# Kernel optimization log

Hardware: AMD Instinct MI355X
Metric: run time of the kernel (lower is better)

The kernel has to match this reference:

```python
import jax, jax.numpy as jnp
import numpy as np

E = 64      # embedding_dim
H = 64      # h_dim
MLP = 1024  # mlp_dim (attention hidden)
PRE1 = 512  # mlp_pre_pool hidden
BNK = 1024  # bottleneck_dim
S = 256     # num scenes (equal-size groups replacing seq_start_end)
P = 16      # pedestrians per scene
B = S * P   # total batch of pedestrians
T = 8       # obs_len for vx/vy (only last row used)
EPS = 1e-5  # BatchNorm eps


def _bn(x, g, b, m, v):
    # eval-mode BatchNorm1d over the last (feature) axis
    return (x - m) * jax.lax.rsqrt(v + EPS) * g + b


def setup_inputs() -> dict:
    key = jax.random.key(0)
    ks = jax.random.split(key, 24)
    def n(k, shape, s=1.0):
        return jax.random.normal(k, shape, jnp.float32) * s
    return {
        "h_states": n(ks[0], (1, B, H)),
        "end_pos": n(ks[1], (B, 2)),
        "vx": n(ks[2], (T, B)),
        "vy": n(ks[3], (T, B)),
        "W_sp": n(ks[4], (2, E), 0.05), "b_sp": jnp.zeros((E,), jnp.float32),
        "W_vel": n(ks[5], (2, E), 0.05), "b_vel": jnp.zeros((E,), jnp.float32),
        "Wa1": n(ks[6], (2 * E, MLP), 0.05), "ba1": jnp.zeros((MLP,), jnp.float32),
        "ga1": jnp.ones((MLP,), jnp.float32), "bta1": jnp.zeros((MLP,), jnp.float32),
        "ma1": n(ks[7], (MLP,), 0.1), "va1": jax.random.uniform(ks[8], (MLP,), jnp.float32) + 0.5,
        "Wa2": n(ks[9], (MLP, 1), 0.05), "ba2": jnp.zeros((1,), jnp.float32),
        "ga2": jnp.ones((1,), jnp.float32), "bta2": jnp.zeros((1,), jnp.float32),
        "ma2": n(ks[10], (1,), 0.1), "va2": jax.random.uniform(ks[11], (1,), jnp.float32) + 0.5,
        "Wp1": n(ks[12], (E + H, PRE1), 0.05), "bp1": jnp.zeros((PRE1,), jnp.float32),
        "gp1": jnp.ones((PRE1,), jnp.float32), "btp1": jnp.zeros((PRE1,), jnp.float32),
        "mp1": n(ks[13], (PRE1,), 0.1), "vp1": jax.random.uniform(ks[14], (PRE1,), jnp.float32) + 0.5,
        "Wp2": n(ks[15], (PRE1, BNK), 0.05), "bp2": jnp.zeros((BNK,), jnp.float32),
        "gp2": jnp.ones((BNK,), jnp.float32), "btp2": jnp.zeros((BNK,), jnp.float32),
        "mp2": n(ks[16], (BNK,), 0.1), "vp2": jax.random.uniform(ks[17], (BNK,), jnp.float32) + 0.5,
        "num_scenes": S, "num_ped": P,
    }


def _forward(h_states, end_pos, vx, vy, W_sp, b_sp, W_vel, b_vel,
             Wa1, ba1, ga1, bta1, ma1, va1, Wa2, ba2, ga2, bta2, ma2, va2,
             Wp1, bp1, gp1, btp1, mp1, vp1, Wp2, bp2, gp2, btp2, mp2, vp2,
             num_scenes, num_ped):
    Sn, Pn = num_scenes, num_ped
    h = h_states.reshape(-1, H).reshape(Sn, Pn, H)          # per-scene hidden
    pos = end_pos.reshape(Sn, Pn, 2)
    # rel[s,i,j] = pos[s,j] - pos[s,i]  (repeat vs repeat_interleave in torch)
    rel = pos[:, None, :, :] - pos[:, :, None, :]
    rel_emb = rel @ W_sp + b_sp                              # [S,P,P,E]
    vel = jnp.stack([vx[-1], vy[-1]], axis=-1).reshape(Sn, Pn, 2)
    vel_emb = vel @ W_vel + b_vel                            # [S,P,E], indexed by row i
    vel_emb = jnp.broadcast_to(vel_emb[:, :, None, :], (Sn, Pn, Pn, E))
    att_in = jnp.concatenate([rel_emb, vel_emb], axis=-1)    # [S,P,P,2E]
    a = jax.nn.relu(_bn(att_in @ Wa1 + ba1, ga1, bta1, ma1, va1))
    scores = jax.nn.relu(_bn(a @ Wa2 + ba2, ga2, bta2, ma2, va2))  # [S,P,P,1]
    # torch.softmax(scores, dim=1) on an (N,1) tensor: softmax over the size-1
    # feature axis -> identically 1.0. Reproduced faithfully here.
    w = jax.nn.softmax(scores, axis=-1)
    h_rep = jnp.broadcast_to(h[:, None, :, :], (Sn, Pn, Pn, H))   # h[s,j] per (i,j)
    x = jnp.concatenate([rel_emb, h_rep], axis=-1) * (0.05 * w)   # [S,P,P,E+H]
    y = jax.nn.relu(_bn(x @ Wp1 + bp1, gp1, btp1, mp1, vp1))
    y = jax.nn.relu(_bn(y @ Wp2 + bp2, gp2, btp2, mp2, vp2))      # [S,P,P,BNK]
    pool = jnp.max(y, axis=2)                                     # max over neighbors j
    return pool.reshape(Sn * Pn, BNK)


def reference(h_states, end_pos, vx, vy, W_sp, b_sp, W_vel, b_vel,
              Wa1, ba1, ga1, bta1, ma1, va1, Wa2, ba2, ga2, bta2, ma2, va2,
              Wp1, bp1, gp1, btp1, mp1, vp1, Wp2, bp2, gp2, btp2, mp2, vp2,
              num_scenes, num_ped):
    return _forward(h_states, end_pos, vx, vy, W_sp, b_sp, W_vel, b_vel,
                    Wa1, ba1, ga1, bta1, ma1, va1, Wa2, ba2, ga2, bta2, ma2, va2,
                    Wp1, bp1, gp1, btp1, mp1, vp1, Wp2, bp2, gp2, btp2, mp2, vp2,
                    num_scenes, num_ped)
```

## Files before the change

kernel.cpp:

```cpp
#include <hip/hip_runtime.h>
#include <hip/hip_bf16.h>
#include <stdint.h>


typedef __bf16 bf16x8 __attribute__((ext_vector_type(8)));
typedef __bf16 bf16x2 __attribute__((ext_vector_type(2)));
typedef float  f32x4  __attribute__((ext_vector_type(4)));
typedef float  f32x2  __attribute__((ext_vector_type(2)));

#define BP2_OFF 0u
#define BP1_OFF 1048576u
#define MX_OFF  1114112u
#define MY_OFF  1116160u
#define CB_OFF  1118208u
#define SH_OFF  1120256u
#define A2_OFF  1122304u
#define C2_OFF  1126400u

#define Y1_LDS  0
#define HH_LDS  131072
#define MX_LDS  147456
#define MY_LDS  149504
#define PF_LDS  151552
#define LDS_SZ  151680

__device__ __forceinline__ unsigned short f2bf(float f) {
    union { float f; unsigned u; } c; c.f = f;
    unsigned u = c.u;
    return (unsigned short)((u + 0x7fffu + ((u >> 16) & 1u)) >> 16);
}
__device__ __forceinline__ float bfbits2f(unsigned hi) {
    union { unsigned u; float f; } c; c.u = hi; return c.f;
}
__device__ __forceinline__ unsigned pk_bf16(float a, float b) {
#if __has_builtin(__builtin_amdgcn_cvt_pk_bf16_f32)
    bf16x2 p = __builtin_amdgcn_cvt_pk_bf16_f32(a, b);
    union { bf16x2 v; unsigned u; } c; c.v = p; return c.u;
#else
    return (unsigned)f2bf(a) | ((unsigned)f2bf(b) << 16);
#endif
}
__device__ __forceinline__ int y1off(int r, int c16) {
    return r * 1024 + (((c16 ^ (c16 >> 3) ^ (r & 7)) & 63) << 4);
}

__global__ __launch_bounds__(256) void prep_pack_kernel(
    const float* __restrict__ Wsp,  const float* __restrict__ bsp,
    const float* __restrict__ Wp1,  const float* __restrict__ bp1,
    const float* __restrict__ gp1,  const float* __restrict__ btp1,
    const float* __restrict__ mp1,  const float* __restrict__ vp1,
    const float* __restrict__ Wp2,  const float* __restrict__ bp2,
    const float* __restrict__ gp2,  const float* __restrict__ btp2,
    const float* __restrict__ mp2,  const float* __restrict__ vp2,
    unsigned char* __restrict__ ws)
{
    __shared__ float tile[32 * 65];
    const int blk = blockIdx.x, t = threadIdx.x;

    if (blk < 272) {
        const float* src; int ncols, kb, ng, KB; unsigned outoff;
        if (blk < 256) { kb = blk >> 4; ng = blk & 15; src = Wp2; ncols = 1024; KB = 16; outoff = BP2_OFF; }
        else { int b2 = blk - 256; kb = b2 >> 3; ng = b2 & 7; src = Wp1 + 64 * 512; ncols = 512; KB = 2; outoff = BP1_OFF; }
        const int k0 = kb * 32, n0 = ng * 64;
        #pragma unroll
        for (int it = 0; it < 2; ++it) {
            int c = t + it * 256;
            int r = c >> 4, c4 = c & 15;
            float4 v = *(const float4*)(src + (k0 + r) * ncols + n0 + c4 * 4);
            tile[r * 65 + c4 * 4 + 0] = v.x;
            tile[r * 65 + c4 * 4 + 1] = v.y;
            tile[r * 65 + c4 * 4 + 2] = v.z;
            tile[r * 65 + c4 * 4 + 3] = v.w;
        }
        __syncthreads();
        int ntl = t >> 6, l = t & 63;
        int nl = ntl * 16 + (l & 15), kl = (l >> 4) * 8;
        uint4 o;
        o.x = pk_bf16(tile[(kl + 0) * 65 + nl], tile[(kl + 1) * 65 + nl]);
        o.y = pk_bf16(tile[(kl + 2) * 65 + nl], tile[(kl + 3) * 65 + nl]);
        o.z = pk_bf16(tile[(kl + 4) * 65 + nl], tile[(kl + 5) * 65 + nl]);
        o.w = pk_bf16(tile[(kl + 6) * 65 + nl], tile[(kl + 7) * 65 + nl]);
        ((uint4*)(ws + outoff))[((ng * 4 + ntl) * KB + kb) * 64 + l] = o;
    } else if (blk < 274) {
        int k = (blk - 272) * 256 + t;
        float a1 = gp1[k] * rsqrtf(vp1[k] + 1e-5f);
        float mx = 0.f, my = 0.f, cb = 0.f;
        for (int e = 0; e < 64; ++e) {
            float wv = Wp1[e * 512 + k];
            mx = fmaf(Wsp[e],      wv, mx);
            my = fmaf(Wsp[64 + e], wv, my);
            cb = fmaf(bsp[e],      wv, cb);
        }
        ((float*)(ws + MX_OFF))[k] = 0.05f * a1 * mx;
        ((float*)(ws + MY_OFF))[k] = 0.05f * a1 * my;
        ((float*)(ws + CB_OFF))[k] = 0.05f * a1 * cb + (bp1[k] - mp1[k]) * a1 + btp1[k];
        ((float*)(ws + SH_OFF))[k] = 0.05f * a1;
    } else {
        int n = (blk - 274) * 256 + t;
        float a = gp2[n] * rsqrtf(vp2[n] + 1e-5f);
        ((float*)(ws + A2_OFF))[n] = a;
        ((float*)(ws + C2_OFF))[n] = btp2[n] + (bp2[n] - mp2[n]) * a;
    }
}

__global__ __launch_bounds__(512, 2) void mm2_kernel(
    const float* __restrict__ hst,
    const float* __restrict__ epos,
    const unsigned char* __restrict__ ws,
    float* __restrict__ out)
{
    __shared__ __align__(16) unsigned char smem[LDS_SZ];
    float* posf = (float*)(smem + PF_LDS);

    const int s   = blockIdx.x >> 1;
    const int ih  = blockIdx.x & 1;
    const int tid = threadIdx.x;
    const int w    = tid >> 6;
    const int l    = tid & 63;
    const int quad = l >> 4;
    const int jl   = l & 15;

    ((float*)(smem + MX_LDS))[tid] = ((const float*)(ws + MX_OFF))[tid];
    ((float*)(smem + MY_LDS))[tid] = ((const float*)(ws + MY_OFF))[tid];
    if (tid < 32) posf[tid] = epos[s * 32 + tid];
    {
        union { unsigned u[4]; bf16x8 v; } afh[2];
        #pragma unroll
        for (int kb = 0; kb < 2; ++kb) {
            const float4* hp = (const float4*)(hst + (s * 16 + jl) * 64 + kb * 32 + quad * 8);
            float4 v0 = hp[0], v1 = hp[1];
            afh[kb].u[0] = pk_bf16(v0.x, v0.y);
            afh[kb].u[1] = pk_bf16(v0.z, v0.w);
            afh[kb].u[2] = pk_bf16(v1.x, v1.y);
            afh[kb].u[3] = pk_bf16(v1.z, v1.w);
        }
        const f32x4 fz = {0.f, 0.f, 0.f, 0.f};
        f32x4 acch[4] = {fz, fz, fz, fz};
        #pragma unroll
        for (int kb = 0; kb < 2; ++kb) {
            #pragma unroll
            for (int ct = 0; ct < 4; ++ct) {
                bf16x8 bfr = *(const bf16x8*)(ws + BP1_OFF + ((((w * 4 + ct) * 2 + kb) * 64 + l) << 4));
                acch[ct] = __builtin_amdgcn_mfma_f32_16x16x32_bf16(afh[kb].v, bfr, acch[ct], 0, 0, 0);
            }
        }
        const float* SHg = (const float*)(ws + SH_OFF);
        const float* CBg = (const float*)(ws + CB_OFF);
        #pragma unroll
        for (int ct = 0; ct < 4; ++ct) {
            int col = (w * 4 + ct) * 16 + jl;
            float sh = SHg[col], cb = CBg[col];
            #pragma unroll
            for (int reg = 0; reg < 4; ++reg) {
                int j = quad * 4 + reg;
                float hv = fmaf(acch[ct][reg], sh, cb);
                *(unsigned short*)(smem + HH_LDS + j * 1024 + col * 2) = f2bf(hv);
            }
        }
    }
    __syncthreads();

    {
        const int i2 = tid >> 8;
        const int j  = (tid >> 4) & 15;
        const int kc = tid & 15;
        float rx[4], ry[4];
        float pjx = posf[j * 2], pjy = posf[j * 2 + 1];
        #pragma unroll
        for (int ii = 0; ii < 4; ++ii) {
            int ig_ = ih * 8 + i2 * 4 + ii;
            rx[ii] = pjx - posf[ig_ * 2];
            ry[ii] = pjy - posf[ig_ * 2 + 1];
        }
        const f32x2 zero2 = {0.f, 0.f};
        #pragma unroll
        for (int kk = 0; kk < 4; ++kk) {
            int k = kc * 32 + kk * 8;
            uint4 hh8 = *(const uint4*)(smem + HH_LDS + j * 1024 + k * 2);
            f32x4 mx0 = *(const f32x4*)(smem + MX_LDS + k * 4);
            f32x4 mx1 = *(const f32x4*)(smem + MX_LDS + k * 4 + 16);
            f32x4 my0 = *(const f32x4*)(smem + MY_LDS + k * 4);
            f32x4 my1 = *(const f32x4*)(smem + MY_LDS + k * 4 + 16);
            f32x2 mxp[4] = { {mx0[0],mx0[1]}, {mx0[2],mx0[3]}, {mx1[0],mx1[1]}, {mx1[2],mx1[3]} };
            f32x2 myp[4] = { {my0[0],my0[1]}, {my0[2],my0[3]}, {my1[0],my1[1]}, {my1[2],my1[3]} };
            f32x2 hhp[4];
            hhp[0][0] = bfbits2f(hh8.x << 16); hhp[0][1] = bfbits2f(hh8.x & 0xffff0000u);
            hhp[1][0] = bfbits2f(hh8.y << 16); hhp[1][1] = bfbits2f(hh8.y & 0xffff0000u);
            hhp[2][0] = bfbits2f(hh8.z << 16); hhp[2][1] = bfbits2f(hh8.z & 0xffff0000u);
            hhp[3][0] = bfbits2f(hh8.w << 16); hhp[3][1] = bfbits2f(hh8.w & 0xffff0000u);
            #pragma unroll
            for (int ii = 0; ii < 4; ++ii) {
                f32x2 rx2 = { rx[ii], rx[ii] };
                f32x2 ry2 = { ry[ii], ry[ii] };
                uint4 o;
                unsigned uu[4];
                #pragma unroll
                for (int p = 0; p < 4; ++p) {
                    f32x2 tt = __builtin_elementwise_fma(ry2, myp[p], hhp[p]);
                    tt = __builtin_elementwise_fma(rx2, mxp[p], tt);
                    tt = __builtin_elementwise_max(tt, zero2);
                    uu[p] = pk_bf16(tt[0], tt[1]);
                }
                o.x = uu[0]; o.y = uu[1]; o.z = uu[2]; o.w = uu[3];
                int r = (i2 * 4 + ii) * 16 + j;
                *(uint4*)(smem + Y1_LDS + y1off(r, kc * 4 + kk)) = o;
            }
        }
    }
    __syncthreads();

    const int ig = w & 1;
    const int ng = w >> 1;
    const float* A2 = (const float*)(ws + A2_OFF);
    const float* C2 = (const float*)(ws + C2_OFF);
    const f32x4 fzero = {0.f, 0.f, 0.f, 0.f};

    #pragma unroll 1
    for (int chunk = 0; chunk < 2; ++chunk) {
        const int ntbase = ng * 16 + chunk * 8;
        const unsigned char* bbase = ws + BP2_OFF + (((size_t)(ntbase * 16) * 64 + l) << 4);
        f32x4 acc[4][8];
        #pragma unroll
        for (int rt = 0; rt < 4; ++rt)
            #pragma unroll
            for (int ct = 0; ct < 8; ++ct) acc[rt][ct] = fzero;

        bf16x8 bcur[8];
        #pragma unroll
        for (int ct = 0; ct < 8; ++ct)
            bcur[ct] = *(const bf16x8*)(bbase + ct * 16384);

        #pragma unroll 1
        for (int ks = 0; ks < 16; ++ks) {
            bf16x8 af[4];
            #pragma unroll
            for (int rt = 0; rt < 4; ++rt) {
                int r = (ig * 4 + rt) * 16 + jl;
                af[rt] = *(const bf16x8*)(smem + Y1_LDS + y1off(r, ks * 4 + quad));
            }
            bf16x8 bnxt[8];
            if (ks < 15) {
                #pragma unroll
                for (int ct = 0; ct < 8; ++ct)
                    bnxt[ct] = *(const bf16x8*)(bbase + (ks + 1) * 1024 + ct * 16384);
            }
            #pragma unroll
            for (int rt = 0; rt < 4; ++rt)
                #pragma unroll
                for (int ct = 0; ct < 8; ++ct)
                    acc[rt][ct] = __builtin_amdgcn_mfma_f32_16x16x32_bf16(af[rt], bcur[ct], acc[rt][ct], 0, 0, 0);
            if (ks < 15) {
                #pragma unroll
                for (int ct = 0; ct < 8; ++ct) bcur[ct] = bnxt[ct];
            }
        }

        #pragma unroll
        for (int ct = 0; ct < 8; ++ct) {
            int col = (ntbase + ct) * 16 + jl;
            float a2 = A2[col], c2 = C2[col];
            #pragma unroll
            for (int rt = 0; rt < 4; ++rt) {
                float v0 = fmaxf(fmaf(acc[rt][ct][0], a2, c2), 0.f);
                float v1 = fmaxf(fmaf(acc[rt][ct][1], a2, c2), 0.f);
                float v2 = fmaxf(fmaf(acc[rt][ct][2], a2, c2), 0.f);
                float v3 = fmaxf(fmaf(acc[rt][ct][3], a2, c2), 0.f);
                float v = fmaxf(fmaxf(v0, v1), fmaxf(v2, v3));
                v = fmaxf(v, __shfl_xor(v, 16, 64));
                v = fmaxf(v, __shfl_xor(v, 32, 64));
                if (l < 16) {
                    int orow = s * 16 + ih * 8 + ig * 4 + rt;
                    __builtin_nontemporal_store(v, &out[orow * 1024 + col]);
                }
            }
        }
    }
}

extern "C" void kernel_launch(void* const* d_in, const int* in_sizes, int n_in,
                              void* d_out, int out_size, void* d_ws, size_t ws_size,
                              hipStream_t stream) {
    const float* hst  = (const float*)d_in[0];
    const float* epos = (const float*)d_in[1];
    const float* Wsp  = (const float*)d_in[4];
    const float* bsp  = (const float*)d_in[5];
    const float* Wp1  = (const float*)d_in[20];
    const float* bp1  = (const float*)d_in[21];
    const float* gp1  = (const float*)d_in[22];
    const float* btp1 = (const float*)d_in[23];
    const float* mp1  = (const float*)d_in[24];
    const float* vp1  = (const float*)d_in[25];
    const float* Wp2  = (const float*)d_in[26];
    const float* bp2  = (const float*)d_in[27];
    const float* gp2  = (const float*)d_in[28];
    const float* btp2 = (const float*)d_in[29];
    const float* mp2  = (const float*)d_in[30];
    const float* vp2  = (const float*)d_in[31];
    unsigned char* ws = (unsigned char*)d_ws;
    float* out = (float*)d_out;

    prep_pack_kernel<<<278, 256, 0, stream>>>(Wsp, bsp, Wp1, bp1, gp1, btp1, mp1, vp1,
                                              Wp2, bp2, gp2, btp2, mp2, vp2, ws);
    mm2_kernel<<<512, 512, 0, stream>>>(hst, epos, ws, out);
}
```

Baseline: 198.4 us.

## Repack Wp2 k-major and double-buffer B fragments in the second GEMM loop

The prep kernel now packs the Wp2 bf16 fragments with k-block outermost, so the 8 column tiles needed per k-step sit contiguously. The main GEMM loop is unrolled by two k-steps, with ping-pong B register buffers so the next global loads are issued while MFMAs on the current step run. The Y1 LDS swizzle is simplified so A-fragment addresses are precomputed once and advanced with a constant stride and an XOR. The MX/MY coefficients and positions are no longer staged in LDS and are read straight from global memory. The last prefetch reads just past the Wp2 region into other workspace data, and dropping the LDS staging adds global traffic in the elementwise phase.

```diff
diff --git a/kernel.cpp b/kernel.cpp
--- a/kernel.cpp
+++ b/kernel.cpp
@@ -19,10 +19,7 @@
 
 #define Y1_LDS  0
 #define HH_LDS  131072
-#define MX_LDS  147456
-#define MY_LDS  149504
-#define PF_LDS  151552
-#define LDS_SZ  151680
+#define LDS_SZ  147456
 
 __device__ __forceinline__ unsigned short f2bf(float f) {
     union { float f; unsigned u; } c; c.f = f;
@@ -41,7 +38,7 @@
 #endif
 }
 __device__ __forceinline__ int y1off(int r, int c16) {
-    return r * 1024 + (((c16 ^ (c16 >> 3) ^ (r & 7)) & 63) << 4);
+    return r * 1024 + ((c16 ^ (r & 7)) << 4);
 }
 
 __global__ __launch_bounds__(256) void prep_pack_kernel(
@@ -58,9 +55,9 @@
     const int blk = blockIdx.x, t = threadIdx.x;
 
     if (blk < 272) {
-        const float* src; int ncols, kb, ng, KB; unsigned outoff;
-        if (blk < 256) { kb = blk >> 4; ng = blk & 15; src = Wp2; ncols = 1024; KB = 16; outoff = BP2_OFF; }
-        else { int b2 = blk - 256; kb = b2 >> 3; ng = b2 & 7; src = Wp1 + 64 * 512; ncols = 512; KB = 2; outoff = BP1_OFF; }
+        const float* src; int ncols, kb, ng;
+        if (blk < 256) { kb = blk >> 4; ng = blk & 15; src = Wp2; ncols = 1024; }
+        else { int b2 = blk - 256; kb = b2 >> 3; ng = b2 & 7; src = Wp1 + 64 * 512; ncols = 512; }
         const int k0 = kb * 32, n0 = ng * 64;
         #pragma unroll
         for (int it = 0; it < 2; ++it) {
@@ -80,7 +77,11 @@
         o.y = pk_bf16(tile[(kl + 2) * 65 + nl], tile[(kl + 3) * 65 + nl]);
         o.z = pk_bf16(tile[(kl + 4) * 65 + nl], tile[(kl + 5) * 65 + nl]);
         o.w = pk_bf16(tile[(kl + 6) * 65 + nl], tile[(kl + 7) * 65 + nl]);
-        ((uint4*)(ws + outoff))[((ng * 4 + ntl) * KB + kb) * 64 + l] = o;
+        if (blk < 256) {
+            ((uint4*)(ws + BP2_OFF))[(kb * 64 + ng * 4 + ntl) * 64 + l] = o;
+        } else {
+            ((uint4*)(ws + BP1_OFF))[((ng * 4 + ntl) * 2 + kb) * 64 + l] = o;
+        }
     } else if (blk < 274) {
         int k = (blk - 272) * 256 + t;
         float a1 = gp1[k] * rsqrtf(vp1[k] + 1e-5f);
@@ -110,7 +111,6 @@
     float* __restrict__ out)
 {
     __shared__ __align__(16) unsigned char smem[LDS_SZ];
-    float* posf = (float*)(smem + PF_LDS);
 
     const int s   = blockIdx.x >> 1;
     const int ih  = blockIdx.x & 1;
@@ -120,9 +120,6 @@
     const int quad = l >> 4;
     const int jl   = l & 15;
 
-    ((float*)(smem + MX_LDS))[tid] = ((const float*)(ws + MX_OFF))[tid];
-    ((float*)(smem + MY_LDS))[tid] = ((const float*)(ws + MY_OFF))[tid];
-    if (tid < 32) posf[tid] = epos[s * 32 + tid];
     {
         union { unsigned u[4]; bf16x8 v; } afh[2];
         #pragma unroll
@@ -165,22 +162,22 @@
         const int j  = (tid >> 4) & 15;
         const int kc = tid & 15;
         float rx[4], ry[4];
-        float pjx = posf[j * 2], pjy = posf[j * 2 + 1];
+        float pjx = epos[s * 32 + j * 2], pjy = epos[s * 32 + j * 2 + 1];
         #pragma unroll
         for (int ii = 0; ii < 4; ++ii) {
             int ig_ = ih * 8 + i2 * 4 + ii;
-            rx[ii] = pjx - posf[ig_ * 2];
-            ry[ii] = pjy - posf[ig_ * 2 + 1];
+            rx[ii] = pjx - epos[s * 32 + ig_ * 2];
+            ry[ii] = pjy - epos[s * 32 + ig_ * 2 + 1];
         }
         const f32x2 zero2 = {0.f, 0.f};
         #pragma unroll
         for (int kk = 0; kk < 4; ++kk) {
             int k = kc * 32 + kk * 8;
             uint4 hh8 = *(const uint4*)(smem + HH_LDS + j * 1024 + k * 2);
-            f32x4 mx0 = *(const f32x4*)(smem + MX_LDS + k * 4);
-            f32x4 mx1 = *(const f32x4*)(smem + MX_LDS + k * 4 + 16);
-            f32x4 my0 = *(const f32x4*)(smem + MY_LDS + k * 4);
-            f32x4 my1 = *(const f32x4*)(smem + MY_LDS + k * 4 + 16);
+            f32x4 mx0 = *(const f32x4*)(ws + MX_OFF + k * 4);
+            f32x4 mx1 = *(const f32x4*)(ws + MX_OFF + k * 4 + 16);
+            f32x4 my0 = *(const f32x4*)(ws + MY_OFF + k * 4);
+            f32x4 my1 = *(const f32x4*)(ws + MY_OFF + k * 4 + 16);
             f32x2 mxp[4] = { {mx0[0],mx0[1]}, {mx0[2],mx0[3]}, {mx1[0],mx1[1]}, {mx1[2],mx1[3]} };
             f32x2 myp[4] = { {my0[0],my0[1]}, {my0[2],my0[3]}, {my1[0],my1[1]}, {my1[2],my1[3]} };
             f32x2 hhp[4];
@@ -215,44 +212,54 @@
     const float* C2 = (const float*)(ws + C2_OFF);
     const f32x4 fzero = {0.f, 0.f, 0.f, 0.f};
 
+    int ab[4];
+    #pragma unroll
+    for (int rt = 0; rt < 4; ++rt) {
+        int r = (ig * 4 + rt) * 16 + jl;
+        ab[rt] = Y1_LDS + r * 1024 + ((quad ^ (r & 7)) << 4);
+    }
+
     #pragma unroll 1
     for (int chunk = 0; chunk < 2; ++chunk) {
         const int ntbase = ng * 16 + chunk * 8;
-        const unsigned char* bbase = ws + BP2_OFF + (((size_t)(ntbase * 16) * 64 + l) << 4);
+        const unsigned char* bp0 = ws + BP2_OFF + (ntbase << 10) + (l << 4);
+
         f32x4 acc[4][8];
         #pragma unroll
         for (int rt = 0; rt < 4; ++rt)
             #pragma unroll
             for (int ct = 0; ct < 8; ++ct) acc[rt][ct] = fzero;
 
-        bf16x8 bcur[8];
+        bf16x8 b0[8], b1[8];
         #pragma unroll
         for (int ct = 0; ct < 8; ++ct)
-            bcur[ct] = *(const bf16x8*)(bbase + ct * 16384);
+            b0[ct] = *(const bf16x8*)(bp0 + ct * 1024);
 
         #pragma unroll 1
-        for (int ks = 0; ks < 16; ++ks) {
-            bf16x8 af[4];
-            #pragma unroll
-            for (int rt = 0; rt < 4; ++rt) {
-                int r = (ig * 4 + rt) * 16 + jl;
-                af[rt] = *(const bf16x8*)(smem + Y1_LDS + y1off(r, ks * 4 + quad));
-            }
-            bf16x8 bnxt[8];
-            if (ks < 15) {
-                #pragma unroll
-                for (int ct = 0; ct < 8; ++ct)
-                    bnxt[ct] = *(const bf16x8*)(bbase + (ks + 1) * 1024 + ct * 16384);
-            }
+        for (int t = 0; t < 8; ++t) {
+            bf16x8 ae[4], ao[4];
+            #pragma unroll
+            for (int rt = 0; rt < 4; ++rt)
+                ae[rt] = *(const bf16x8*)(smem + (ab[rt] + t * 128));
+            #pragma unroll
+            for (int ct = 0; ct < 8; ++ct)
+                b1[ct] = *(const bf16x8*)(bp0 + (2 * t + 1) * 65536 + ct * 1024);
+            #pragma unroll
+            for (int rt = 0; rt < 4; ++rt)
+                ao[rt] = *(const bf16x8*)(smem + ((ab[rt] + t * 128) ^ 64));
             #pragma unroll
             for (int rt = 0; rt < 4; ++rt)
                 #pragma unroll
                 for (int ct = 0; ct < 8; ++ct)
-                    acc[rt][ct] = __builtin_amdgcn_mfma_f32_16x16x32_bf16(af[rt], bcur[ct], acc[rt][ct], 0, 0, 0);
-            if (ks < 15) {
+                    acc[rt][ct] = __builtin_amdgcn_mfma_f32_16x16x32_bf16(ae[rt], b0[ct], acc[rt][ct], 0, 0, 0);
+            #pragma unroll
+            for (int ct = 0; ct < 8; ++ct)
+                b0[ct] = *(const bf16x8*)(bp0 + (2 * t + 2) * 65536 + ct * 1024);
+            #pragma unroll
+            for (int rt = 0; rt < 4; ++rt)
                 #pragma unroll
-                for (int ct = 0; ct < 8; ++ct) bcur[ct] = bnxt[ct];
-            }
+                for (int ct = 0; ct < 8; ++ct)
+                    acc[rt][ct] = __builtin_amdgcn_mfma_f32_16x16x32_bf16(ao[rt], b1[ct], acc[rt][ct], 0, 0, 0);
         }
 
         #pragma unroll
```

After: 196.7 us. About the same (-0.9%).
